# Kernel tuning notes

Measured on AMD Instinct MI355X. Metric: run time of the kernel, lower is better.

The kernel has to match this reference:

```python
import jax, jax.numpy as jnp
import numpy as np

DT = 0.01
NJ = 7
GRAV = 9.81
Q_LOWER = jnp.array([-2.9671, -1.8326, -2.9671, -3.1416, -2.9671, -0.0873, -2.9671], jnp.float32)
Q_UPPER = jnp.array([ 2.9671,  1.8326,  2.9671,  0.0,     2.9671,  3.8223,  2.9671], jnp.float32)


def _skew(v):
    z = jnp.zeros((), v.dtype)
    return jnp.stack([jnp.stack([z, -v[2], v[1]]),
                      jnp.stack([v[2], z, -v[0]]),
                      jnp.stack([-v[1], v[0], z])])


def _mot_X(E, r):
    # 6x6 spatial motion transform [[E,0],[-E*skew(r),E]]
    zero = jnp.zeros_like(E)
    top = jnp.concatenate([E, zero], axis=1)
    bot = jnp.concatenate([-E @ _skew(r), E], axis=1)
    return jnp.concatenate([top, bot], axis=0)


def _crm(v):
    # spatial motion cross-product matrix for v=[w;v0]
    Sw, Sv = _skew(v[:3]), _skew(v[3:])
    zero = jnp.zeros_like(Sw)
    top = jnp.concatenate([Sw, zero], axis=1)
    bot = jnp.concatenate([Sv, Sw], axis=1)
    return jnp.concatenate([top, bot], axis=0)


def _step_single(x, u, axes, R_tree, p_tree, I_sp):
    dt_ = x.dtype
    q = jnp.clip(x[:NJ], Q_LOWER.astype(dt_), Q_UPPER.astype(dt_))
    qd = x[NJ:]
    # forward kinematics: per-joint 6x6 child<-parent transforms and motion subspaces
    Xups, Ss = [], []
    eye3 = jnp.eye(3, dtype=dt_)
    for i in range(NJ):
        a = axes[i]
        c, s = jnp.cos(q[i]), jnp.sin(q[i])
        R = c * eye3 + s * _skew(a) + (1.0 - c) * jnp.outer(a, a)  # rodrigues
        Xj = _mot_X(R.T, jnp.zeros(3, dt_))
        Xt = _mot_X(R_tree[i], p_tree[i])
        Xups.append(Xj @ Xt)
        Ss.append(jnp.concatenate([a, jnp.zeros(3, dt_)]))
    # RNEA bias force h (qdd=0, gravity, zero base velocity, identity base pose)
    v_prev = jnp.zeros(6, dt_)
    a_prev = jnp.array([0.0, 0.0, 0.0, 0.0, 0.0, GRAV], dt_)  # a_base = -g trick
    fs = []
    for i in range(NJ):
        vJ = Ss[i] * qd[i]
        v = Xups[i] @ v_prev + vJ
        acc = Xups[i] @ a_prev + _crm(v) @ vJ
        Iv = I_sp[i] @ v
        f = I_sp[i] @ acc - _crm(v).T @ Iv  # crf(v) = -crm(v)^T
        fs.append(f)
        v_prev, a_prev = v, acc
    h = [None] * NJ
    for i in range(NJ - 1, -1, -1):
        h[i] = Ss[i] @ fs[i]
        if i > 0:
            fs[i - 1] = fs[i - 1] + Xups[i].T @ fs[i]
    h = jnp.stack(h)
    # CRBA mass matrix (serial chain, parent(i)=i-1)
    Ic = [I_sp[i] for i in range(NJ)]
    M = jnp.zeros((NJ, NJ), dt_)
    for i in range(NJ - 1, -1, -1):
        if i > 0:
            Ic[i - 1] = Ic[i - 1] + Xups[i].T @ Ic[i] @ Xups[i]
        F = Ic[i] @ Ss[i]
        M = M.at[i, i].set(Ss[i] @ F)
        for j in range(i - 1, -1, -1):
            F = Xups[j + 1].T @ F
            mij = Ss[j] @ F
            M = M.at[i, j].set(mij).at[j, i].set(mij)
    M = M + 1e-8 * jnp.eye(NJ, dtype=dt_)
    qdd = jnp.linalg.solve(M, (u - h)[:, None])[:, 0]
    qd_new = qd + DT * qdd
    q_new = q + DT * qd_new
    return jnp.concatenate([q_new, qd_new])


def setup_inputs() -> dict:
    B = 65536
    key = jax.random.key(0)
    k1, k2 = jax.random.split(key)
    x = jax.random.normal(k1, (B, 14), jnp.float32)
    u = jax.random.normal(k2, (B, 7), jnp.float32)
    rng = np.random.default_rng(0)
    # unit joint axes
    axes = rng.normal(size=(NJ, 3))
    axes = axes / np.linalg.norm(axes, axis=1, keepdims=True)
    # orthonormal fixed parent->child rotations (det +1)
    R_tree = np.empty((NJ, 3, 3))
    for i in range(NJ):
        Q, _ = np.linalg.qr(rng.normal(size=(3, 3)))
        if np.linalg.det(Q) < 0:
            Q[:, 0] = -Q[:, 0]
        R_tree[i] = Q
    p_tree = 0.2 * rng.normal(size=(NJ, 3))
    # SPD 6x6 spatial inertias: [[Ibar, m*Cx],[m*Cx^T, m*I3]]
    I_sp = np.empty((NJ, 6, 6))
    for i in range(NJ):
        m = float(rng.uniform(1.0, 5.0))
        c = 0.05 * rng.normal(size=3)
        Cx = np.array([[0, -c[2], c[1]], [c[2], 0, -c[0]], [-c[1], c[0], 0]])
        A = 0.1 * rng.normal(size=(3, 3))
        Ic_ = A @ A.T + 0.05 * np.eye(3)
        Ibar = Ic_ + m * Cx @ Cx.T
        I_sp[i] = np.block([[Ibar, m * Cx], [m * Cx.T, m * np.eye(3)]])
    return {
        "x": x, "u": u,
        "axes": jnp.asarray(axes, jnp.float32),
        "R_tree": jnp.asarray(R_tree, jnp.float32),
        "p_tree": jnp.asarray(p_tree, jnp.float32),
        "I_sp": jnp.asarray(I_sp, jnp.float32),
    }


def reference(x, u, axes, R_tree, p_tree, I_sp):
    return jax.vmap(_step_single, in_axes=(0, 0, None, None, None, None))(
        x, u, axes, R_tree, p_tree, I_sp)
```

## Files before the change

### kernel.cpp

```cpp
#include <hip/hip_runtime.h>
#include <math.h>

#define NJ 7
#define DTF 0.01f
#define GRAVF 9.81f
#define MIX(i,j) ((i)*((i)+1)/2 + (j))

__device__ __forceinline__ void cross3(const float* a, const float* b, float* o){
    o[0] = a[1]*b[2] - a[2]*b[1];
    o[1] = a[2]*b[0] - a[0]*b[2];
    o[2] = a[0]*b[1] - a[1]*b[0];
}
__device__ __forceinline__ void mv3(const float* E, const float* x, float* y){
    y[0] = E[0]*x[0] + E[1]*x[1] + E[2]*x[2];
    y[1] = E[3]*x[0] + E[4]*x[1] + E[5]*x[2];
    y[2] = E[6]*x[0] + E[7]*x[1] + E[8]*x[2];
}
__device__ __forceinline__ void mtv3(const float* E, const float* x, float* y){
    y[0] = E[0]*x[0] + E[3]*x[1] + E[6]*x[2];
    y[1] = E[1]*x[0] + E[4]*x[1] + E[7]*x[2];
    y[2] = E[2]*x[0] + E[5]*x[1] + E[8]*x[2];
}
__device__ __forceinline__ void mm3(const float* A, const float* B, float* o){
#pragma unroll
    for (int r = 0; r < 3; r++){
#pragma unroll
        for (int c = 0; c < 3; c++){
            o[r*3+c] = A[r*3]*B[c] + A[r*3+1]*B[3+c] + A[r*3+2]*B[6+c];
        }
    }
}
__device__ __forceinline__ void congr(const float* E, const float* X, float* o){
    float t[9];
#pragma unroll
    for (int r = 0; r < 3; r++){
#pragma unroll
        for (int c = 0; c < 3; c++){
            t[r*3+c] = E[r]*X[c] + E[3+r]*X[3+c] + E[6+r]*X[6+c];
        }
    }
    mm3(t, E, o);
}

__global__ __launch_bounds__(256)
void panda_step(const float* __restrict__ x, const float* __restrict__ u,
                const float* __restrict__ g_ax, const float* __restrict__ g_Rt,
                const float* __restrict__ g_pt, const float* __restrict__ g_I,
                float* __restrict__ out, int B)
{
    __shared__ float s_ax[NJ*3], s_Rt[NJ*9], s_pt[NJ*3], s_A[NJ*9], s_h[NJ*3], s_m[NJ];
    if (threadIdx.x < NJ){
        int i = threadIdx.x;
#pragma unroll
        for (int k = 0; k < 3; k++){ s_ax[i*3+k] = g_ax[i*3+k]; s_pt[i*3+k] = g_pt[i*3+k]; }
#pragma unroll
        for (int k = 0; k < 9; k++) s_Rt[i*9+k] = g_Rt[i*9+k];
        const float* I6 = g_I + i*36;
#pragma unroll
        for (int r = 0; r < 3; r++)
#pragma unroll
            for (int c = 0; c < 3; c++) s_A[i*9+r*3+c] = I6[r*6+c];
        s_h[i*3+0] = I6[2*6+3+1];
        s_h[i*3+1] = I6[0*6+3+2];
        s_h[i*3+2] = I6[1*6+3+0];
        s_m[i]     = I6[3*6+3];
    }
    __syncthreads();

    int b = blockIdx.x*blockDim.x + threadIdx.x;
    if (b >= B) return;

    const float QL[NJ] = {-2.9671f,-1.8326f,-2.9671f,-3.1416f,-2.9671f,-0.0873f,-2.9671f};
    const float QU[NJ] = { 2.9671f, 1.8326f, 2.9671f, 0.0f,    2.9671f, 3.8223f, 2.9671f};

    float xl[14];
    {
        const float2* x2 = (const float2*)(x + b*14);
#pragma unroll
        for (int i = 0; i < 7; i++){ float2 v = x2[i]; xl[2*i] = v.x; xl[2*i+1] = v.y; }
    }
    float q[NJ], qd[NJ], sn[NJ], cs[NJ];
#pragma unroll
    for (int i = 0; i < NJ; i++){
        q[i]  = fminf(fmaxf(xl[i], QL[i]), QU[i]);
        qd[i] = xl[NJ + i];
        __sincosf(q[i], &sn[i], &cs[i]);
    }
    float rhs[NJ];
#pragma unroll
    for (int i = 0; i < NJ; i++) rhs[i] = u[b*NJ + i];

    auto makeE = [&](int i, float* Eo){
        const float* a = &s_ax[i*3];
        float s = sn[i], c = cs[i], omc = 1.0f - c;
        float RT[9];
        RT[0] = c + omc*a[0]*a[0];       RT[1] =  s*a[2] + omc*a[0]*a[1]; RT[2] = -s*a[1] + omc*a[0]*a[2];
        RT[3] = -s*a[2] + omc*a[1]*a[0]; RT[4] = c + omc*a[1]*a[1];       RT[5] =  s*a[0] + omc*a[1]*a[2];
        RT[6] =  s*a[1] + omc*a[2]*a[0]; RT[7] = -s*a[0] + omc*a[2]*a[1]; RT[8] = c + omc*a[2]*a[2];
        mm3(RT, &s_Rt[i*9], Eo);
    };

    float FF[NJ][6];
    float w[3]  = {0.f,0.f,0.f}, vl[3] = {0.f,0.f,0.f};
    float aw[3] = {0.f,0.f,0.f}, av[3] = {0.f,0.f,GRAVF};
#pragma unroll
    for (int i = 0; i < NJ; i++){
        const float* a = &s_ax[i*3];
        const float* p = &s_pt[i*3];
        float E[9]; makeE(i, E);
        float qdi = qd[i];
        float tw[3]; mv3(E, w, tw);
        float nw[3] = { tw[0]+a[0]*qdi, tw[1]+a[1]*qdi, tw[2]+a[2]*qdi };
        float cwp[3]; cross3(w, p, cwp);
        float t1[3] = { vl[0]+cwp[0], vl[1]+cwp[1], vl[2]+cwp[2] };
        float nvl[3]; mv3(E, t1, nvl);
        float taw[3]; mv3(E, aw, taw);
        float cna[3]; cross3(nw, a, cna);
        float naw[3] = { taw[0]+qdi*cna[0], taw[1]+qdi*cna[1], taw[2]+qdi*cna[2] };
        float cap[3]; cross3(aw, p, cap);
        float t2[3] = { av[0]+cap[0], av[1]+cap[1], av[2]+cap[2] };
        float tav[3]; mv3(E, t2, tav);
        float cva[3]; cross3(nvl, a, cva);
        float nav[3] = { tav[0]+qdi*cva[0], tav[1]+qdi*cva[1], tav[2]+qdi*cva[2] };
        const float* Ai = &s_A[i*9];
        const float* hi = &s_h[i*3];
        float mi = s_m[i];
        float Ivt[3], Iat[3], hxv[3], hxa[3];
        mv3(Ai, nw, Ivt);  cross3(hi, nvl, hxv);
        mv3(Ai, naw, Iat); cross3(hi, nav, hxa);
#pragma unroll
        for (int k = 0; k < 3; k++){ Ivt[k] += hxv[k]; Iat[k] += hxa[k]; }
        float hxw[3], hxaw[3];
        cross3(hi, nw, hxw); cross3(hi, naw, hxaw);
        float Ivb[3] = { mi*nvl[0]-hxw[0], mi*nvl[1]-hxw[1], mi*nvl[2]-hxw[2] };
        float Iab[3] = { mi*nav[0]-hxaw[0], mi*nav[1]-hxaw[1], mi*nav[2]-hxaw[2] };
        float c1[3], c2[3], c3[3];
        cross3(nw, Ivt, c1); cross3(nvl, Ivb, c2); cross3(nw, Ivb, c3);
        FF[i][0] = Iat[0]+c1[0]+c2[0];
        FF[i][1] = Iat[1]+c1[1]+c2[1];
        FF[i][2] = Iat[2]+c1[2]+c2[2];
        FF[i][3] = Iab[0]+c3[0];
        FF[i][4] = Iab[1]+c3[1];
        FF[i][5] = Iab[2]+c3[2];
#pragma unroll
        for (int k = 0; k < 3; k++){ w[k]=nw[k]; vl[k]=nvl[k]; aw[k]=naw[k]; av[k]=nav[k]; }
    }

    float SA[6], hc[3], mc;
    {
        const float* A6 = &s_A[6*9];
        SA[0]=A6[0]; SA[1]=A6[1]; SA[2]=A6[2]; SA[3]=A6[4]; SA[4]=A6[5]; SA[5]=A6[8];
        hc[0]=s_h[18]; hc[1]=s_h[19]; hc[2]=s_h[20];
        mc = s_m[6];
    }
    float Mx[28];
#pragma unroll
    for (int i = NJ-1; i >= 0; i--){
        const float* a = &s_ax[i*3];
        const float* p = &s_pt[i*3];
        float E[9]; makeE(i, E);
        rhs[i] -= a[0]*FF[i][0] + a[1]*FF[i][1] + a[2]*FF[i][2];
        if (i > 0){
            float tm[3], tf[3], cp[3];
            mtv3(E, &FF[i][0], tm); mtv3(E, &FF[i][3], tf);
            cross3(p, tf, cp);
            FF[i-1][0]+=tm[0]+cp[0]; FF[i-1][1]+=tm[1]+cp[1]; FF[i-1][2]+=tm[2]+cp[2];
            FF[i-1][3]+=tf[0];       FF[i-1][4]+=tf[1];       FF[i-1][5]+=tf[2];
        }
        FF[i][0] = SA[0]*a[0] + SA[1]*a[1] + SA[2]*a[2];
        FF[i][1] = SA[1]*a[0] + SA[3]*a[1] + SA[4]*a[2];
        FF[i][2] = SA[2]*a[0] + SA[4]*a[1] + SA[5]*a[2];
        FF[i][3] = a[1]*hc[2] - a[2]*hc[1];
        FF[i][4] = a[2]*hc[0] - a[0]*hc[2];
        FF[i][5] = a[0]*hc[1] - a[1]*hc[0];
        Mx[MIX(i,i)] = a[0]*FF[i][0] + a[1]*FF[i][1] + a[2]*FF[i][2];
#pragma unroll
        for (int k = i+1; k < NJ; k++)
            Mx[MIX(k,i)] = a[0]*FF[k][0] + a[1]*FF[k][1] + a[2]*FF[k][2];
        if (i > 0){
            float Af[9] = {SA[0],SA[1],SA[2], SA[1],SA[3],SA[4], SA[2],SA[4],SA[5]};
            float Ap[9]; congr(E, Af, Ap);
            float hr[3]; mtv3(E, hc, hr);
            float hpd = hr[0]*p[0]+hr[1]*p[1]+hr[2]*p[2];
            float ppd = p[0]*p[0]+p[1]*p[1]+p[2]*p[2];
            float dga = 2.0f*hpd + mc*ppd;
            const float* An = &s_A[(i-1)*9];
            SA[0] = Ap[0] - 2.0f*p[0]*hr[0] - mc*p[0]*p[0] + dga + An[0];
            SA[1] = Ap[1] - p[0]*hr[1] - hr[0]*p[1] - mc*p[0]*p[1] + An[1];
            SA[2] = Ap[2] - p[0]*hr[2] - hr[0]*p[2] - mc*p[0]*p[2] + An[2];
            SA[3] = Ap[4] - 2.0f*p[1]*hr[1] - mc*p[1]*p[1] + dga + An[4];
            SA[4] = Ap[5] - p[1]*hr[2] - hr[1]*p[2] - mc*p[1]*p[2] + An[5];
            SA[5] = Ap[8] - 2.0f*p[2]*hr[2] - mc*p[2]*p[2] + dga + An[8];
            hc[0] = hr[0] + mc*p[0] + s_h[(i-1)*3+0];
            hc[1] = hr[1] + mc*p[1] + s_h[(i-1)*3+1];
            hc[2] = hr[2] + mc*p[2] + s_h[(i-1)*3+2];
            mc += s_m[i-1];
#pragma unroll
            for (int k = i; k < NJ; k++){
                float tm[3], tf[3], cp[3];
                mtv3(E, &FF[k][0], tm); mtv3(E, &FF[k][3], tf);
                cross3(p, tf, cp);
                FF[k][0]=tm[0]+cp[0]; FF[k][1]=tm[1]+cp[1]; FF[k][2]=tm[2]+cp[2];
                FF[k][3]=tf[0];       FF[k][4]=tf[1];       FF[k][5]=tf[2];
            }
        }
    }
#pragma unroll
    for (int i = 0; i < NJ; i++) Mx[MIX(i,i)] += 1e-8f;

#pragma unroll
    for (int k = 0; k < NJ; k++){
        float d = Mx[MIX(k,k)];
#pragma unroll
        for (int j = 0; j < NJ; j++) if (j < k) d -= Mx[MIX(k,j)]*Mx[MIX(k,j)];
        float linv = __builtin_amdgcn_rsqf(d);
        Mx[MIX(k,k)] = linv;
#pragma unroll
        for (int i = k+1; i < NJ; i++){
            float s2 = Mx[MIX(i,k)];
#pragma unroll
            for (int j = 0; j < NJ; j++) if (j < k) s2 -= Mx[MIX(i,j)]*Mx[MIX(k,j)];
            Mx[MIX(i,k)] = s2 * linv;
        }
    }
    float y[NJ];
#pragma unroll
    for (int i = 0; i < NJ; i++){
        float s2 = rhs[i];
#pragma unroll
        for (int j = 0; j < NJ; j++) if (j < i) s2 -= Mx[MIX(i,j)]*y[j];
        y[i] = s2 * Mx[MIX(i,i)];
    }
    float z[NJ];
#pragma unroll
    for (int i = NJ-1; i >= 0; i--){
        float s2 = y[i];
#pragma unroll
        for (int j = NJ-1; j >= 0; j--) if (j > i) s2 -= Mx[MIX(j,i)]*z[j];
        z[i] = s2 * Mx[MIX(i,i)];
    }

    float o14[14];
#pragma unroll
    for (int i = 0; i < NJ; i++){
        float qdn = qd[i] + DTF*z[i];
        o14[i]      = q[i] + DTF*qdn;
        o14[NJ + i] = qdn;
    }
    float2* o2 = (float2*)(out + b*14);
#pragma unroll
    for (int i = 0; i < 7; i++){ float2 v; v.x = o14[2*i]; v.y = o14[2*i+1]; o2[i] = v; }
}

extern "C" void kernel_launch(void* const* d_in, const int* in_sizes, int n_in,
                              void* d_out, int out_size, void* d_ws, size_t ws_size,
                              hipStream_t stream) {
    const float* x   = (const float*)d_in[0];
    const float* u   = (const float*)d_in[1];
    const float* ax  = (const float*)d_in[2];
    const float* Rt  = (const float*)d_in[3];
    const float* pt  = (const float*)d_in[4];
    const float* Isp = (const float*)d_in[5];
    float* out = (float*)d_out;
    int B = in_sizes[0] / 14;
    int block = 256;
    int grid = (B + block - 1) / block;
    hipLaunchKernelGGL(panda_step, dim3(grid), dim3(block), 0, stream,
                       x, u, ax, Rt, pt, Isp, out, B);
}
```

Measured before the change: 92.67 us.

## Split RNEA and CRBA across two wavefronts per batch element via LDS

Each block now handles 64 batch elements with two wavefronts: one computes the RNEA bias force and rhs, the other computes the CRBA mass matrix and writes it to padded shared memory. After a barrier, the first wavefront loads the matrix, does the Cholesky solve and writes the output. This halves the serial per-thread work and register pressure, at the cost of duplicated sincos and FK work, twice the threads, and an LDS round trip plus a barrier.

```diff
diff --git a/kernel.cpp b/kernel.cpp
--- a/kernel.cpp
+++ b/kernel.cpp
@@ -5,6 +5,7 @@
 #define DTF 0.01f
 #define GRAVF 9.81f
 #define MIX(i,j) ((i)*((i)+1)/2 + (j))
+#define MPAD 29
 
 __device__ __forceinline__ void cross3(const float* a, const float* b, float* o){
     o[0] = a[1]*b[2] - a[2]*b[1];
@@ -41,14 +42,24 @@
     }
     mm3(t, E, o);
 }
-
-__global__ __launch_bounds__(256)
+__device__ __forceinline__ void makeE(const float* a, float s, float c,
+                                      const float* Rt, float* Eo){
+    float omc = 1.0f - c;
+    float RT[9];
+    RT[0] = c + omc*a[0]*a[0];       RT[1] =  s*a[2] + omc*a[0]*a[1]; RT[2] = -s*a[1] + omc*a[0]*a[2];
+    RT[3] = -s*a[2] + omc*a[1]*a[0]; RT[4] = c + omc*a[1]*a[1];       RT[5] =  s*a[0] + omc*a[1]*a[2];
+    RT[6] =  s*a[1] + omc*a[2]*a[0]; RT[7] = -s*a[0] + omc*a[2]*a[1]; RT[8] = c + omc*a[2]*a[2];
+    mm3(RT, Rt, Eo);
+}
+
+__global__ __launch_bounds__(128)
 void panda_step(const float* __restrict__ x, const float* __restrict__ u,
                 const float* __restrict__ g_ax, const float* __restrict__ g_Rt,
                 const float* __restrict__ g_pt, const float* __restrict__ g_I,
                 float* __restrict__ out, int B)
 {
     __shared__ float s_ax[NJ*3], s_Rt[NJ*9], s_pt[NJ*3], s_A[NJ*9], s_h[NJ*3], s_m[NJ];
+    __shared__ float s_M[64*MPAD];
     if (threadIdx.x < NJ){
         int i = threadIdx.x;
 #pragma unroll
@@ -67,189 +78,201 @@
     }
     __syncthreads();
 
-    int b = blockIdx.x*blockDim.x + threadIdx.x;
-    if (b >= B) return;
+    const int role = threadIdx.x >> 6;
+    const int lane = threadIdx.x & 63;
+    const int e    = blockIdx.x*64 + lane;
+    const bool act = (e < B);
 
     const float QL[NJ] = {-2.9671f,-1.8326f,-2.9671f,-3.1416f,-2.9671f,-0.0873f,-2.9671f};
     const float QU[NJ] = { 2.9671f, 1.8326f, 2.9671f, 0.0f,    2.9671f, 3.8223f, 2.9671f};
 
-    float xl[14];
-    {
-        const float2* x2 = (const float2*)(x + b*14);
+    float q[NJ], qd[NJ], sn[NJ], cs[NJ];
+    if (act){
+        float xl[14];
+        const float2* x2 = (const float2*)(x + e*14);
 #pragma unroll
         for (int i = 0; i < 7; i++){ float2 v = x2[i]; xl[2*i] = v.x; xl[2*i+1] = v.y; }
-    }
-    float q[NJ], qd[NJ], sn[NJ], cs[NJ];
-#pragma unroll
-    for (int i = 0; i < NJ; i++){
-        q[i]  = fminf(fmaxf(xl[i], QL[i]), QU[i]);
-        qd[i] = xl[NJ + i];
-        __sincosf(q[i], &sn[i], &cs[i]);
-    }
+#pragma unroll
+        for (int i = 0; i < NJ; i++){
+            q[i]  = fminf(fmaxf(xl[i], QL[i]), QU[i]);
+            qd[i] = xl[NJ + i];
+            __sincosf(q[i], &sn[i], &cs[i]);
+        }
+    }
+
     float rhs[NJ];
-#pragma unroll
-    for (int i = 0; i < NJ; i++) rhs[i] = u[b*NJ + i];
-
-    auto makeE = [&](int i, float* Eo){
-        const float* a = &s_ax[i*3];
-        float s = sn[i], c = cs[i], omc = 1.0f - c;
-        float RT[9];
-        RT[0] = c + omc*a[0]*a[0];       RT[1] =  s*a[2] + omc*a[0]*a[1]; RT[2] = -s*a[1] + omc*a[0]*a[2];
-        RT[3] = -s*a[2] + omc*a[1]*a[0]; RT[4] = c + omc*a[1]*a[1];       RT[5] =  s*a[0] + omc*a[1]*a[2];
-        RT[6] =  s*a[1] + omc*a[2]*a[0]; RT[7] = -s*a[0] + omc*a[2]*a[1]; RT[8] = c + omc*a[2]*a[2];
-        mm3(RT, &s_Rt[i*9], Eo);
-    };
-
-    float FF[NJ][6];
-    float w[3]  = {0.f,0.f,0.f}, vl[3] = {0.f,0.f,0.f};
-    float aw[3] = {0.f,0.f,0.f}, av[3] = {0.f,0.f,GRAVF};
-#pragma unroll
-    for (int i = 0; i < NJ; i++){
-        const float* a = &s_ax[i*3];
-        const float* p = &s_pt[i*3];
-        float E[9]; makeE(i, E);
-        float qdi = qd[i];
-        float tw[3]; mv3(E, w, tw);
-        float nw[3] = { tw[0]+a[0]*qdi, tw[1]+a[1]*qdi, tw[2]+a[2]*qdi };
-        float cwp[3]; cross3(w, p, cwp);
-        float t1[3] = { vl[0]+cwp[0], vl[1]+cwp[1], vl[2]+cwp[2] };
-        float nvl[3]; mv3(E, t1, nvl);
-        float taw[3]; mv3(E, aw, taw);
-        float cna[3]; cross3(nw, a, cna);
-        float naw[3] = { taw[0]+qdi*cna[0], taw[1]+qdi*cna[1], taw[2]+qdi*cna[2] };
-        float cap[3]; cross3(aw, p, cap);
-        float t2[3] = { av[0]+cap[0], av[1]+cap[1], av[2]+cap[2] };
-        float tav[3]; mv3(E, t2, tav);
-        float cva[3]; cross3(nvl, a, cva);
-        float nav[3] = { tav[0]+qdi*cva[0], tav[1]+qdi*cva[1], tav[2]+qdi*cva[2] };
-        const float* Ai = &s_A[i*9];
-        const float* hi = &s_h[i*3];
-        float mi = s_m[i];
-        float Ivt[3], Iat[3], hxv[3], hxa[3];
-        mv3(Ai, nw, Ivt);  cross3(hi, nvl, hxv);
-        mv3(Ai, naw, Iat); cross3(hi, nav, hxa);
-#pragma unroll
-        for (int k = 0; k < 3; k++){ Ivt[k] += hxv[k]; Iat[k] += hxa[k]; }
-        float hxw[3], hxaw[3];
-        cross3(hi, nw, hxw); cross3(hi, naw, hxaw);
-        float Ivb[3] = { mi*nvl[0]-hxw[0], mi*nvl[1]-hxw[1], mi*nvl[2]-hxw[2] };
-        float Iab[3] = { mi*nav[0]-hxaw[0], mi*nav[1]-hxaw[1], mi*nav[2]-hxaw[2] };
-        float c1[3], c2[3], c3[3];
-        cross3(nw, Ivt, c1); cross3(nvl, Ivb, c2); cross3(nw, Ivb, c3);
-        FF[i][0] = Iat[0]+c1[0]+c2[0];
-        FF[i][1] = Iat[1]+c1[1]+c2[1];
-        FF[i][2] = Iat[2]+c1[2]+c2[2];
-        FF[i][3] = Iab[0]+c3[0];
-        FF[i][4] = Iab[1]+c3[1];
-        FF[i][5] = Iab[2]+c3[2];
-#pragma unroll
-        for (int k = 0; k < 3; k++){ w[k]=nw[k]; vl[k]=nvl[k]; aw[k]=naw[k]; av[k]=nav[k]; }
-    }
-
-    float SA[6], hc[3], mc;
-    {
-        const float* A6 = &s_A[6*9];
-        SA[0]=A6[0]; SA[1]=A6[1]; SA[2]=A6[2]; SA[3]=A6[4]; SA[4]=A6[5]; SA[5]=A6[8];
-        hc[0]=s_h[18]; hc[1]=s_h[19]; hc[2]=s_h[20];
-        mc = s_m[6];
-    }
-    float Mx[28];
-#pragma unroll
-    for (int i = NJ-1; i >= 0; i--){
-        const float* a = &s_ax[i*3];
-        const float* p = &s_pt[i*3];
-        float E[9]; makeE(i, E);
-        rhs[i] -= a[0]*FF[i][0] + a[1]*FF[i][1] + a[2]*FF[i][2];
-        if (i > 0){
-            float tm[3], tf[3], cp[3];
-            mtv3(E, &FF[i][0], tm); mtv3(E, &FF[i][3], tf);
-            cross3(p, tf, cp);
-            FF[i-1][0]+=tm[0]+cp[0]; FF[i-1][1]+=tm[1]+cp[1]; FF[i-1][2]+=tm[2]+cp[2];
-            FF[i-1][3]+=tf[0];       FF[i-1][4]+=tf[1];       FF[i-1][5]+=tf[2];
-        }
-        FF[i][0] = SA[0]*a[0] + SA[1]*a[1] + SA[2]*a[2];
-        FF[i][1] = SA[1]*a[0] + SA[3]*a[1] + SA[4]*a[2];
-        FF[i][2] = SA[2]*a[0] + SA[4]*a[1] + SA[5]*a[2];
-        FF[i][3] = a[1]*hc[2] - a[2]*hc[1];
-        FF[i][4] = a[2]*hc[0] - a[0]*hc[2];
-        FF[i][5] = a[0]*hc[1] - a[1]*hc[0];
-        Mx[MIX(i,i)] = a[0]*FF[i][0] + a[1]*FF[i][1] + a[2]*FF[i][2];
-#pragma unroll
-        for (int k = i+1; k < NJ; k++)
-            Mx[MIX(k,i)] = a[0]*FF[k][0] + a[1]*FF[k][1] + a[2]*FF[k][2];
-        if (i > 0){
-            float Af[9] = {SA[0],SA[1],SA[2], SA[1],SA[3],SA[4], SA[2],SA[4],SA[5]};
-            float Ap[9]; congr(E, Af, Ap);
-            float hr[3]; mtv3(E, hc, hr);
-            float hpd = hr[0]*p[0]+hr[1]*p[1]+hr[2]*p[2];
-            float ppd = p[0]*p[0]+p[1]*p[1]+p[2]*p[2];
-            float dga = 2.0f*hpd + mc*ppd;
-            const float* An = &s_A[(i-1)*9];
-            SA[0] = Ap[0] - 2.0f*p[0]*hr[0] - mc*p[0]*p[0] + dga + An[0];
-            SA[1] = Ap[1] - p[0]*hr[1] - hr[0]*p[1] - mc*p[0]*p[1] + An[1];
-            SA[2] = Ap[2] - p[0]*hr[2] - hr[0]*p[2] - mc*p[0]*p[2] + An[2];
-            SA[3] = Ap[4] - 2.0f*p[1]*hr[1] - mc*p[1]*p[1] + dga + An[4];
-            SA[4] = Ap[5] - p[1]*hr[2] - hr[1]*p[2] - mc*p[1]*p[2] + An[5];
-            SA[5] = Ap[8] - 2.0f*p[2]*hr[2] - mc*p[2]*p[2] + dga + An[8];
-            hc[0] = hr[0] + mc*p[0] + s_h[(i-1)*3+0];
-            hc[1] = hr[1] + mc*p[1] + s_h[(i-1)*3+1];
-            hc[2] = hr[2] + mc*p[2] + s_h[(i-1)*3+2];
-            mc += s_m[i-1];
-#pragma unroll
-            for (int k = i; k < NJ; k++){
+
+    if (act && role == 1){
+        float SA[6], hc[3], mc;
+        {
+            const float* A6 = &s_A[6*9];
+            SA[0]=A6[0]; SA[1]=A6[1]; SA[2]=A6[2]; SA[3]=A6[4]; SA[4]=A6[5]; SA[5]=A6[8];
+            hc[0]=s_h[18]; hc[1]=s_h[19]; hc[2]=s_h[20];
+            mc = s_m[6];
+        }
+        float Fk[NJ][6];
+        float Mx[28];
+#pragma unroll
+        for (int i = NJ-1; i >= 0; i--){
+            const float* a = &s_ax[i*3];
+            const float* p = &s_pt[i*3];
+            Fk[i][0] = SA[0]*a[0] + SA[1]*a[1] + SA[2]*a[2];
+            Fk[i][1] = SA[1]*a[0] + SA[3]*a[1] + SA[4]*a[2];
+            Fk[i][2] = SA[2]*a[0] + SA[4]*a[1] + SA[5]*a[2];
+            Fk[i][3] = a[1]*hc[2] - a[2]*hc[1];
+            Fk[i][4] = a[2]*hc[0] - a[0]*hc[2];
+            Fk[i][5] = a[0]*hc[1] - a[1]*hc[0];
+#pragma unroll
+            for (int k = i; k < NJ; k++)
+                Mx[MIX(k,i)] = a[0]*Fk[k][0] + a[1]*Fk[k][1] + a[2]*Fk[k][2];
+            if (i > 0){
+                float E[9]; makeE(a, sn[i], cs[i], &s_Rt[i*9], E);
+                float Af[9] = {SA[0],SA[1],SA[2], SA[1],SA[3],SA[4], SA[2],SA[4],SA[5]};
+                float Ap[9]; congr(E, Af, Ap);
+                float hr[3]; mtv3(E, hc, hr);
+                float hpd = hr[0]*p[0]+hr[1]*p[1]+hr[2]*p[2];
+                float ppd = p[0]*p[0]+p[1]*p[1]+p[2]*p[2];
+                float dga = 2.0f*hpd + mc*ppd;
+                const float* An = &s_A[(i-1)*9];
+                SA[0] = Ap[0] - 2.0f*p[0]*hr[0] - mc*p[0]*p[0] + dga + An[0];
+                SA[1] = Ap[1] - p[0]*hr[1] - hr[0]*p[1] - mc*p[0]*p[1] + An[1];
+                SA[2] = Ap[2] - p[0]*hr[2] - hr[0]*p[2] - mc*p[0]*p[2] + An[2];
+                SA[3] = Ap[4] - 2.0f*p[1]*hr[1] - mc*p[1]*p[1] + dga + An[4];
+                SA[4] = Ap[5] - p[1]*hr[2] - hr[1]*p[2] - mc*p[1]*p[2] + An[5];
+                SA[5] = Ap[8] - 2.0f*p[2]*hr[2] - mc*p[2]*p[2] + dga + An[8];
+                hc[0] = hr[0] + mc*p[0] + s_h[(i-1)*3+0];
+                hc[1] = hr[1] + mc*p[1] + s_h[(i-1)*3+1];
+                hc[2] = hr[2] + mc*p[2] + s_h[(i-1)*3+2];
+                mc += s_m[i-1];
+#pragma unroll
+                for (int k = i; k < NJ; k++){
+                    float tm[3], tf[3], cp[3];
+                    mtv3(E, &Fk[k][0], tm); mtv3(E, &Fk[k][3], tf);
+                    cross3(p, tf, cp);
+                    Fk[k][0]=tm[0]+cp[0]; Fk[k][1]=tm[1]+cp[1]; Fk[k][2]=tm[2]+cp[2];
+                    Fk[k][3]=tf[0];       Fk[k][4]=tf[1];       Fk[k][5]=tf[2];
+                }
+            }
+        }
+#pragma unroll
+        for (int j = 0; j < 28; j++) s_M[lane*MPAD + j] = Mx[j];
+    }
+    else if (act){
+#pragma unroll
+        for (int i = 0; i < NJ; i++) rhs[i] = u[e*NJ + i];
+        float FF[NJ][6];
+        float w[3]  = {0.f,0.f,0.f}, vl[3] = {0.f,0.f,0.f};
+        float aw[3] = {0.f,0.f,0.f}, av[3] = {0.f,0.f,GRAVF};
+#pragma unroll
+        for (int i = 0; i < NJ; i++){
+            const float* a = &s_ax[i*3];
+            const float* p = &s_pt[i*3];
+            float E[9]; makeE(a, sn[i], cs[i], &s_Rt[i*9], E);
+            float qdi = qd[i];
+            float tw[3]; mv3(E, w, tw);
+            float nw[3] = { tw[0]+a[0]*qdi, tw[1]+a[1]*qdi, tw[2]+a[2]*qdi };
+            float cwp[3]; cross3(w, p, cwp);
+            float t1[3] = { vl[0]+cwp[0], vl[1]+cwp[1], vl[2]+cwp[2] };
+            float nvl[3]; mv3(E, t1, nvl);
+            float taw[3]; mv3(E, aw, taw);
+            float cna[3]; cross3(nw, a, cna);
+            float naw[3] = { taw[0]+qdi*cna[0], taw[1]+qdi*cna[1], taw[2]+qdi*cna[2] };
+            float cap[3]; cross3(aw, p, cap);
+            float t2[3] = { av[0]+cap[0], av[1]+cap[1], av[2]+cap[2] };
+            float tav[3]; mv3(E, t2, tav);
+            float cva[3]; cross3(nvl, a, cva);
+            float nav[3] = { tav[0]+qdi*cva[0], tav[1]+qdi*cva[1], tav[2]+qdi*cva[2] };
+            const float* Ai = &s_A[i*9];
+            const float* hi = &s_h[i*3];
+            float mi = s_m[i];
+            float Ivt[3], Iat[3], hxv[3], hxa[3];
+            mv3(Ai, nw, Ivt);  cross3(hi, nvl, hxv);
+            mv3(Ai, naw, Iat); cross3(hi, nav, hxa);
+#pragma unroll
+            for (int k = 0; k < 3; k++){ Ivt[k] += hxv[k]; Iat[k] += hxa[k]; }
+            float hxw[3], hxaw[3];
+            cross3(hi, nw, hxw); cross3(hi, naw, hxaw);
+            float Ivb[3] = { mi*nvl[0]-hxw[0], mi*nvl[1]-hxw[1], mi*nvl[2]-hxw[2] };
+            float Iab[3] = { mi*nav[0]-hxaw[0], mi*nav[1]-hxaw[1], mi*nav[2]-hxaw[2] };
+            float c1[3], c2[3], c3[3];
+            cross3(nw, Ivt, c1); cross3(nvl, Ivb, c2); cross3(nw, Ivb, c3);
+            FF[i][0] = Iat[0]+c1[0]+c2[0];
+            FF[i][1] = Iat[1]+c1[1]+c2[1];
+            FF[i][2] = Iat[2]+c1[2]+c2[2];
+            FF[i][3] = Iab[0]+c3[0];
+            FF[i][4] = Iab[1]+c3[1];
+            FF[i][5] = Iab[2]+c3[2];
+#pragma unroll
+            for (int k = 0; k < 3; k++){ w[k]=nw[k]; vl[k]=nvl[k]; aw[k]=naw[k]; av[k]=nav[k]; }
+        }
+#pragma unroll
+        for (int i = NJ-1; i >= 0; i--){
+            const float* a = &s_ax[i*3];
+            rhs[i] -= a[0]*FF[i][0] + a[1]*FF[i][1] + a[2]*FF[i][2];
+            if (i > 0){
+                const float* p = &s_pt[i*3];
+                float E[9]; makeE(a, sn[i], cs[i], &s_Rt[i*9], E);
                 float tm[3], tf[3], cp[3];
-                mtv3(E, &FF[k][0], tm); mtv3(E, &FF[k][3], tf);
+                mtv3(E, &FF[i][0], tm); mtv3(E, &FF[i][3], tf);
                 cross3(p, tf, cp);
-                FF[k][0]=tm[0]+cp[0]; FF[k][1]=tm[1]+cp[1]; FF[k][2]=tm[2]+cp[2];
-                FF[k][3]=tf[0];       FF[k][4]=tf[1];       FF[k][5]=tf[2];
+                FF[i-1][0]+=tm[0]+cp[0]; FF[i-1][1]+=tm[1]+cp[1]; FF[i-1][2]+=tm[2]+cp[2];
+                FF[i-1][3]+=tf[0];       FF[i-1][4]+=tf[1];       FF[i-1][5]+=tf[2];
             }
         }
     }
-#pragma unroll
-    for (int i = 0; i < NJ; i++) Mx[MIX(i,i)] += 1e-8f;
-
-#pragma unroll
-    for (int k = 0; k < NJ; k++){
-        float d = Mx[MIX(k,k)];
-#pragma unroll
-        for (int j = 0; j < NJ; j++) if (j < k) d -= Mx[MIX(k,j)]*Mx[MIX(k,j)];
-        float linv = __builtin_amdgcn_rsqf(d);
-        Mx[MIX(k,k)] = linv;
-#pragma unroll
-        for (int i = k+1; i < NJ; i++){
-            float s2 = Mx[MIX(i,k)];
-#pragma unroll
-            for (int j = 0; j < NJ; j++) if (j < k) s2 -= Mx[MIX(i,j)]*Mx[MIX(k,j)];
-            Mx[MIX(i,k)] = s2 * linv;
-        }
-    }
-    float y[NJ];
-#pragma unroll
-    for (int i = 0; i < NJ; i++){
-        float s2 = rhs[i];
-#pragma unroll
-        for (int j = 0; j < NJ; j++) if (j < i) s2 -= Mx[MIX(i,j)]*y[j];
-        y[i] = s2 * Mx[MIX(i,i)];
-    }
-    float z[NJ];
-#pragma unroll
-    for (int i = NJ-1; i >= 0; i--){
-        float s2 = y[i];
-#pragma unroll
-        for (int j = NJ-1; j >= 0; j--) if (j > i) s2 -= Mx[MIX(j,i)]*z[j];
-        z[i] = s2 * Mx[MIX(i,i)];
-    }
-
-    float o14[14];
-#pragma unroll
-    for (int i = 0; i < NJ; i++){
-        float qdn = qd[i] + DTF*z[i];
-        o14[i]      = q[i] + DTF*qdn;
-        o14[NJ + i] = qdn;
-    }
-    float2* o2 = (float2*)(out + b*14);
-#pragma unroll
-    for (int i = 0; i < 7; i++){ float2 v; v.x = o14[2*i]; v.y = o14[2*i+1]; o2[i] = v; }
+
+    __syncthreads();
+
+    if (act && role == 0){
+        float Mx[28];
+#pragma unroll
+        for (int j = 0; j < 28; j++) Mx[j] = s_M[lane*MPAD + j];
+#pragma unroll
+        for (int i = 0; i < NJ; i++) Mx[MIX(i,i)] += 1e-8f;
+
+#pragma unroll
+        for (int k = 0; k < NJ; k++){
+            float d = Mx[MIX(k,k)];
+#pragma unroll
+            for (int j = 0; j < NJ; j++) if (j < k) d -= Mx[MIX(k,j)]*Mx[MIX(k,j)];
+            float linv = __builtin_amdgcn_rsqf(d);
+            Mx[MIX(k,k)] = linv;
+#pragma unroll
+            for (int i = k+1; i < NJ; i++){
+                float s2 = Mx[MIX(i,k)];
+#pragma unroll
+                for (int j = 0; j < NJ; j++) if (j < k) s2 -= Mx[MIX(i,j)]*Mx[MIX(k,j)];
+                Mx[MIX(i,k)] = s2 * linv;
+            }
+        }
+        float y[NJ];
+#pragma unroll
+        for (int i = 0; i < NJ; i++){
+            float s2 = rhs[i];
+#pragma unroll
+            for (int j = 0; j < NJ; j++) if (j < i) s2 -= Mx[MIX(i,j)]*y[j];
+            y[i] = s2 * Mx[MIX(i,i)];
+        }
+        float z[NJ];
+#pragma unroll
+        for (int i = NJ-1; i >= 0; i--){
+            float s2 = y[i];
+#pragma unroll
+            for (int j = NJ-1; j >= 0; j--) if (j > i) s2 -= Mx[MIX(j,i)]*z[j];
+            z[i] = s2 * Mx[MIX(i,i)];
+        }
+
+        float o14[14];
+#pragma unroll
+        for (int i = 0; i < NJ; i++){
+            float qdn = qd[i] + DTF*z[i];
+            o14[i]      = q[i] + DTF*qdn;
+            o14[NJ + i] = qdn;
+        }
+        float2* o2 = (float2*)(out + e*14);
+#pragma unroll
+        for (int i = 0; i < 7; i++){ float2 v; v.x = o14[2*i]; v.y = o14[2*i+1]; o2[i] = v; }
+    }
 }
 
 extern "C" void kernel_launch(void* const* d_in, const int* in_sizes, int n_in,
@@ -263,8 +286,7 @@
     const float* Isp = (const float*)d_in[5];
     float* out = (float*)d_out;
     int B = in_sizes[0] / 14;
-    int block = 256;
-    int grid = (B + block - 1) / block;
-    hipLaunchKernelGGL(panda_step, dim3(grid), dim3(block), 0, stream,
+    int grid = (B + 63) / 64;
+    hipLaunchKernelGGL(panda_step, dim3(grid), dim3(128), 0, stream,
                        x, u, ax, Rt, pt, Isp, out, B);
 }
```

New measurement: 82.67 us. 10.8% less time.
